# Kernel optimization log

Hardware: AMD Instinct MI355X
Metric: run time of the kernel (lower is better)

Reference implementation:

```python
import jax, jax.numpy as jnp
import numpy as np

N = 50000      # num nodes
E = 400000     # num edges
D = 384        # input_dim
H = 4          # heads
C = 128        # hidden_dim per head
HC = H * C     # 512


def setup_inputs() -> dict:
    key = jax.random.key(0)
    ks = jax.random.split(key, 32)
    w = lambda k, shape: jax.random.normal(k, shape, jnp.float32) * 0.05
    inp = {
        "x": jax.random.normal(ks[0], (N, D), jnp.float32),
        "edge_index": jax.random.randint(ks[1], (2, E), 0, N, dtype=jnp.int32),
    }
    dims = [(D, HC), (HC, HC)]  # layer0 in=384, layer1 in=512
    i = 2
    for l, (din, dout) in enumerate(dims):
        for nm in ["q", "k", "v", "s"]:  # query/key/value/skip linears
            inp[f"{nm}{l}_w"] = w(ks[i], (dout, din)); i += 1
            inp[f"{nm}{l}_b"] = jnp.zeros((dout,), jnp.float32)
    inp["out_w"] = w(ks[i], (D, HC))
    inp["out_b"] = jnp.zeros((D,), jnp.float32)
    return inp


def _transformer_conv(x, src, dst, Wq, bq, Wk, bk, Wv, bv, Ws, bs):
    # PyG TransformerConv, concat=True, root_weight=True, no edge features.
    n = x.shape[0]
    q = (x @ Wq.T + bq).reshape(n, H, C)
    k = (x @ Wk.T + bk).reshape(n, H, C)
    v = (x @ Wv.T + bv).reshape(n, H, C)
    # per-edge attention logits [E, H]; target = dst, source = src
    alpha = (q[dst] * k[src]).sum(-1) / jnp.sqrt(jnp.float32(C))
    m = jax.ops.segment_max(alpha, dst, num_segments=n)
    m = jnp.where(jnp.isfinite(m), m, 0.0)  # nodes with no in-edges
    e = jnp.exp(alpha - m[dst])
    denom = jax.ops.segment_sum(e, dst, num_segments=n)
    a = e / (denom[dst] + 1e-16)             # segment softmax [E, H]
    msg = v[src] * a[:, :, None]             # [E, H, C]
    agg = jax.ops.segment_sum(msg, dst, num_segments=n).reshape(n, HC)
    return agg + x @ Ws.T + bs               # + root/skip connection


def reference(x, edge_index,
              q0_w, q0_b, k0_w, k0_b, v0_w, v0_b, s0_w, s0_b,
              q1_w, q1_b, k1_w, k1_b, v1_w, v1_b, s1_w, s1_b,
              out_w, out_b):
    src, dst = edge_index[0], edge_index[1]
    h = _transformer_conv(x, src, dst, q0_w, q0_b, k0_w, k0_b, v0_w, v0_b, s0_w, s0_b)
    h = jax.nn.relu(h)
    h = _transformer_conv(h, src, dst, q1_w, q1_b, k1_w, k1_b, v1_w, v1_b, s1_w, s1_b)
    h = jax.nn.relu(h)
    return h @ out_w.T + out_b  # [N, D]
```

## Files before the change

kernel.cpp:

```cpp
#include <hip/hip_runtime.h>
#include <hip/hip_bf16.h>

#define NN 50000
#define NE 400000
#define DD 384
#define HC 512

typedef unsigned int u32;
typedef unsigned short u16;
typedef __attribute__((ext_vector_type(8))) short bf16x8;
typedef __attribute__((ext_vector_type(4))) float f32x4;

#define AS1 __attribute__((address_space(1)))
#define AS3 __attribute__((address_space(3)))

__device__ __forceinline__ float bflo(u32 u){ return __uint_as_float(u << 16); }
__device__ __forceinline__ float bfhi(u32 u){ return __uint_as_float(u & 0xFFFF0000u); }
__device__ __forceinline__ u16 f2bf(float f){
    u32 u = __float_as_uint(f);
    return (u16)((u + 0x7FFFu + ((u >> 16) & 1u)) >> 16);
}
__device__ __forceinline__ u32 pack2(float a, float b){
    return (u32)f2bf(a) | ((u32)f2bf(b) << 16);
}

template<int K>
__global__ __launch_bounds__(512)
void gemm_ws(const u16* __restrict__ Ab, const u16* __restrict__ Wb,
             const float* __restrict__ bias,
             u16* __restrict__ oQ, u16* __restrict__ oK,
             u16* __restrict__ oV, u16* __restrict__ oS)
{
    constexpr int NKT  = K / 64;
    constexpr int WCH  = K / 8;
    constexpr int NPAN = (NN + 127) / 128;
    __shared__ char smW[128 * K * 2];
    __shared__ char smA[2][16384];

    const int b   = blockIdx.x;
    const int xcd = b & 7;
    const int idx = b >> 3;
    const int ct  = idx & 15;
    const int rh  = idx >> 4;

    const int tid  = threadIdx.x;
    const int lane = tid & 63;
    const int w    = tid >> 6;
    const int wq   = w >> 1;
    const int wc   = w & 1;
    const int r16  = lane & 15;
    const int kq   = lane >> 4;

    {
        const u16* W0 = Wb + (size_t)ct * 128 * K;
        #pragma unroll
        for (int p = 0; p < (128 * WCH) / 512; ++p) {
            int ci = p * 512 + tid;
            int row = ci / WCH, pc = ci % WCH;
            int lc = (pc & ~7) | ((pc ^ row) & 7);
            __builtin_amdgcn_global_load_lds((const AS1 u32*)(W0 + (size_t)row * K + lc * 8),
                                             (AS3 u32*)(smW + (size_t)ci * 16), 16, 0, 0);
        }
    }

    int np = 0;
    while ((2 * np + rh) * 8 + xcd < NPAN) ++np;
    const int total = np * NKT;

    auto stageA = [&](int t) {
        int jp = t / NKT, kc = t - jp * NKT;
        int m0 = ((2 * jp + rh) * 8 + xcd) * 128;
        #pragma unroll
        for (int p = 0; p < 2; ++p) {
            int ci = p * 512 + tid;
            int row = ci >> 3, pc = ci & 7;
            int lc = pc ^ (row & 7);
            int gr = m0 + row; if (gr >= NN) gr = NN - 1;
            __builtin_amdgcn_global_load_lds((const AS1 u32*)(Ab + (size_t)gr * K + kc * 64 + lc * 8),
                                             (AS3 u32*)(smA[t & 1] + ci * 16), 16, 0, 0);
        }
    };

    stageA(0);
    if (total > 1) stageA(1);

    f32x4 acc[2][4] = {};

    const int qsel = ct >> 2;
    u16* outp = (qsel == 0) ? oQ : (qsel == 1) ? oK : (qsel == 2) ? oV : oS;
    const int cb = (ct & 3) * 128 + wc * 64;
    float bb[4][4];
    #pragma unroll
    for (int ni = 0; ni < 4; ++ni)
        #pragma unroll
        for (int r = 0; r < 4; ++r)
            bb[ni][r] = bias[ct * 128 + wc * 64 + ni * 16 + kq * 4 + r];

    for (int t = 0; t < total; ++t) {
        const int jp = t / NKT, kc = t - jp * NKT;
        if (t + 1 >= total)        { asm volatile("s_waitcnt vmcnt(0)"  ::: "memory"); }
        else if (kc == 0 && t > 0) { asm volatile("s_waitcnt vmcnt(10)" ::: "memory"); }
        else                       { asm volatile("s_waitcnt vmcnt(2)"  ::: "memory"); }
        __builtin_amdgcn_s_barrier();
        __builtin_amdgcn_sched_barrier(0);

        const char* bufA = smA[t & 1];
        #pragma unroll
        for (int kk = 0; kk < 2; ++kk) {
            const int slot = (((kk << 2) + kq) ^ (r16 & 7)) << 4;
            bf16x8 av[2], bv[4];
            #pragma unroll
            for (int i = 0; i < 2; ++i)
                av[i] = *(const bf16x8*)(bufA + (wq * 32 + i * 16 + r16) * 128 + slot);
            #pragma unroll
            for (int i = 0; i < 4; ++i) {
                int rw = wc * 64 + i * 16 + r16;
                bv[i] = *(const bf16x8*)(smW + (size_t)rw * (K * 2) + kc * 128 + slot);
            }
            #pragma unroll
            for (int mi = 0; mi < 2; ++mi)
                #pragma unroll
                for (int ni = 0; ni < 4; ++ni)
                    acc[mi][ni] = __builtin_amdgcn_mfma_f32_16x16x32_bf16(
                        bv[ni], av[mi], acc[mi][ni], 0, 0, 0);
        }

        __builtin_amdgcn_sched_barrier(0);
        __builtin_amdgcn_s_barrier();
        __builtin_amdgcn_sched_barrier(0);

        if (kc == NKT - 1) {
            int m0 = ((2 * jp + rh) * 8 + xcd) * 128;
            #pragma unroll
            for (int mi = 0; mi < 2; ++mi) {
                int gr = m0 + wq * 32 + mi * 16 + r16;
                bool ok = gr < NN;
                #pragma unroll
                for (int ni = 0; ni < 4; ++ni) {
                    uint2 o;
                    o.x = pack2(acc[mi][ni][0] + bb[ni][0], acc[mi][ni][1] + bb[ni][1]);
                    o.y = pack2(acc[mi][ni][2] + bb[ni][2], acc[mi][ni][3] + bb[ni][3]);
                    if (ok) *(uint2*)(outp + (size_t)gr * 512 + cb + ni * 16 + kq * 4) = o;
                    #pragma unroll
                    for (int r = 0; r < 4; ++r) acc[mi][ni][r] = 0.f;
                }
            }
        }
        if (t + 2 < total) stageA(t + 2);
    }
}

template<int K>
__global__ __launch_bounds__(256)
void gemm2ph(const u16* __restrict__ Ab, const u16* __restrict__ Wb,
             const float* __restrict__ bias, float* __restrict__ oF,
             int n, int Ototal, int NT)
{
    constexpr int NKT = K / 64;
    __shared__ char smA[2][16384];
    __shared__ char smB[2][16384];

    const int nb  = gridDim.x;
    const int bd  = blockIdx.x;
    const int q8  = nb >> 3, r8 = nb & 7;
    const int xcd = bd & 7, gg = bd >> 3;
    const int tt  = (xcd < r8 ? xcd * (q8 + 1) : r8 * (q8 + 1) + (xcd - r8) * q8) + gg;
    const int m0  = (tt / NT) * 128;
    const int o0  = (tt % NT) * 128;

    const int tid  = threadIdx.x;
    const int lane = tid & 63;
    const int w    = tid >> 6;
    const int wr   = w >> 1, wc = w & 1;
    const int r16  = lane & 15;
    const int kq   = lane >> 4;

    auto stage = [&](int bf, int kt) {
        #pragma unroll
        for (int p = 0; p < 4; ++p) {
            int ci = p * 256 + tid, row = ci >> 3, pc = ci & 7;
            int lc = pc ^ (row & 7);
            const u16* g = Wb + (size_t)(o0 + row) * K + kt * 64 + lc * 8;
            __builtin_amdgcn_global_load_lds((const AS1 u32*)g,
                                             (AS3 u32*)(smB[bf] + ci * 16), 16, 0, 0);
        }
        #pragma unroll
        for (int p = 0; p < 4; ++p) {
            int ci = p * 256 + tid, row = ci >> 3, pc = ci & 7;
            int lc = pc ^ (row & 7);
            int gr = m0 + row; if (gr >= n) gr = n - 1;
            const u16* g = Ab + (size_t)gr * K + kt * 64 + lc * 8;
            __builtin_amdgcn_global_load_lds((const AS1 u32*)g,
                                             (AS3 u32*)(smA[bf] + ci * 16), 16, 0, 0);
        }
    };

    f32x4 acc[4][4] = {};

    stage(0, 0);
    stage(1, 1);

    for (int kt = 0; kt < NKT; ++kt) {
        if (kt + 1 < NKT) { asm volatile("s_waitcnt vmcnt(8)" ::: "memory"); }
        else             { asm volatile("s_waitcnt vmcnt(0)" ::: "memory"); }
        __builtin_amdgcn_s_barrier();
        __builtin_amdgcn_sched_barrier(0);

        const char* pa = smA[kt & 1] + (wr * 64) * 128;
        const char* pb = smB[kt & 1] + (wc * 64) * 128;
        #pragma unroll
        for (int kk = 0; kk < 2; ++kk) {
            const int slot = (((kk << 2) + kq) ^ (r16 & 7)) << 4;
            bf16x8 av[4], bv[4];
            #pragma unroll
            for (int i = 0; i < 4; ++i) {
                av[i] = *(const bf16x8*)(pa + (i * 16 + r16) * 128 + slot);
                bv[i] = *(const bf16x8*)(pb + (i * 16 + r16) * 128 + slot);
            }
            #pragma unroll
            for (int mi = 0; mi < 4; ++mi)
                #pragma unroll
                for (int ni = 0; ni < 4; ++ni)
                    acc[mi][ni] = __builtin_amdgcn_mfma_f32_16x16x32_bf16(
                        bv[ni], av[mi], acc[mi][ni], 0, 0, 0);
        }

        __builtin_amdgcn_sched_barrier(0);
        __builtin_amdgcn_s_barrier();
        __builtin_amdgcn_sched_barrier(0);
        if (kt + 2 < NKT) stage(kt & 1, kt + 2);
    }

    #pragma unroll
    for (int mi = 0; mi < 4; ++mi) {
        int gr = m0 + wr * 64 + mi * 16 + r16;
        if (gr >= n) continue;
        #pragma unroll
        for (int ni = 0; ni < 4; ++ni) {
            int col = o0 + wc * 64 + ni * 16 + kq * 4;
            float4 o = make_float4(acc[mi][ni][0] + bias[col],
                                   acc[mi][ni][1] + bias[col + 1],
                                   acc[mi][ni][2] + bias[col + 2],
                                   acc[mi][ni][3] + bias[col + 3]);
            *(float4*)(oF + (size_t)gr * Ototal + col) = o;
        }
    }
}

#define XG  2400000
#define W0G 24576
#define W1G 32768
#define WOG 24576
#define CVT_TOTAL (XG + 4*W0G + 4*W1G + WOG)

__global__ __launch_bounds__(256)
void cvt_all(const float* __restrict__ x,
             const float* q0w, const float* k0w, const float* v0w, const float* s0w,
             const float* q1w, const float* k1w, const float* v1w, const float* s1w,
             const float* ow,
             u16* __restrict__ Xb, u16* __restrict__ Wc0,
             u16* __restrict__ Wc1, u16* __restrict__ WcO)
{
    int i = blockIdx.x * 256 + threadIdx.x;
    if (i >= CVT_TOTAL) return;
    const float* s; u16* d; int g;
    if (i < XG) { s = x; d = Xb; g = i; }
    else {
        int j = i - XG;
        if (j < 4 * W0G) {
            int q = j / W0G; g = j - q * W0G;
            s = (q == 0 ? q0w : q == 1 ? k0w : q == 2 ? v0w : s0w);
            d = Wc0 + (size_t)q * W0G * 8;
        } else if ((j -= 4 * W0G) < 4 * W1G) {
            int q = j / W1G; g = j - q * W1G;
            s = (q == 0 ? q1w : q == 1 ? k1w : q == 2 ? v1w : s1w);
            d = Wc1 + (size_t)q * W1G * 8;
        } else { j -= 4 * W1G; s = ow; d = WcO; g = j; }
    }
    float4 f0 = ((const float4*)s)[(size_t)g * 2];
    float4 f1 = ((const float4*)s)[(size_t)g * 2 + 1];
    uint4 o;
    o.x = pack2(f0.x, f0.y); o.y = pack2(f0.z, f0.w);
    o.z = pack2(f1.x, f1.y); o.w = pack2(f1.z, f1.w);
    ((uint4*)d)[g] = o;
}

__global__ __launch_bounds__(256)
void pack_bias(const float* q0, const float* k0, const float* v0, const float* s0,
               const float* q1, const float* k1, const float* v1, const float* s1,
               const float* ob, float* __restrict__ dst)
{
    int i = blockIdx.x * 256 + threadIdx.x;
    if (i >= 4480) return;
    float v;
    if (i < 2048) {
        int j = i & 511, q = i >> 9;
        v = (q == 0 ? q0 : q == 1 ? k0 : q == 2 ? v0 : s0)[j];
    } else if (i < 4096) {
        int j = i - 2048; int q = j >> 9; j &= 511;
        v = (q == 0 ? q1 : q == 1 ? k1 : q == 2 ? v1 : s1)[j];
    } else {
        v = ob[i - 4096];
    }
    dst[i] = v;
}

__global__ __launch_bounds__(256)
void zero_deg(int* __restrict__ deg)
{
    int i = blockIdx.x * 256 + threadIdx.x;
    if (i < NN) deg[i] = 0;
}

__global__ __launch_bounds__(256)
void hist_dst(const int* __restrict__ dst, int* __restrict__ deg)
{
    int e = blockIdx.x * 256 + threadIdx.x;
    if (e < NE) atomicAdd(&deg[dst[e]], 1);
}

__global__ __launch_bounds__(1024)
void scan_deg(const int* __restrict__ deg, int* __restrict__ rowptr,
              int* __restrict__ cursor)
{
    __shared__ int wsum[16];
    const int tid = threadIdx.x, lane = tid & 63, wid = tid >> 6;
    int carry = 0;
    for (int base = 0; base < NN; base += 1024) {
        int i = base + tid;
        int orig = (i < NN) ? deg[i] : 0;
        int v = orig;
        #pragma unroll
        for (int off = 1; off < 64; off <<= 1) {
            int t = __shfl_up(v, off, 64);
            if (lane >= off) v += t;
        }
        if (lane == 63) wsum[wid] = v;
        __syncthreads();
        if (wid == 0) {
            int s = (lane < 16) ? wsum[lane] : 0;
            #pragma unroll
            for (int off = 1; off < 16; off <<= 1) {
                int t = __shfl_up(s, off, 16);
                if ((lane & 15) >= off) s += t;
            }
            if (lane < 16) wsum[lane] = s;
        }
        __syncthreads();
        int woff  = (wid == 0) ? 0 : wsum[wid - 1];
        int total = wsum[15];
        int excl  = carry + woff + (v - orig);
        if (i < NN) { rowptr[i] = excl; cursor[i] = excl; }
        carry += total;
        __syncthreads();
    }
    if (tid == 0) rowptr[NN] = NE;
}

__global__ __launch_bounds__(256)
void scatter_edges(const int* __restrict__ src, const int* __restrict__ dst,
                   int* __restrict__ cursor, int* __restrict__ esrc_ord)
{
    int e = blockIdx.x * 256 + threadIdx.x;
    if (e >= NE) return;
    int pos = atomicAdd(&cursor[dst[e]], 1);
    esrc_ord[pos] = src[e];
}

__global__ __launch_bounds__(256)
void node_attn(const u16* __restrict__ Qb, const u16* __restrict__ Kb,
               const u16* __restrict__ Vb, const int* __restrict__ rowptr,
               const int* __restrict__ esrc, const u16* __restrict__ skipb,
               u16* __restrict__ outb)
{
    int d = blockIdx.x * 4 + (threadIdx.x >> 6);
    if (d >= NN) return;
    int lane = threadIdx.x & 63;

    uint4 qv = *((const uint4*)(Qb + (size_t)d * HC) + lane);
    float q[8] = { bflo(qv.x), bfhi(qv.x), bflo(qv.y), bfhi(qv.y),
                   bflo(qv.z), bfhi(qv.z), bflo(qv.w), bfhi(qv.w) };

    int beg = rowptr[d], end = rowptr[d + 1];
    float m = -INFINITY, den = 0.f;
    float acc[8] = {};

    if (beg < end) {
        int s0 = esrc[beg];
        uint4 kv = *((const uint4*)(Kb + (size_t)s0 * HC) + lane);
        uint4 vv = *((const uint4*)(Vb + (size_t)s0 * HC) + lane);

        for (int i = beg; i < end; ++i) {
            uint4 kc = kv, vc = vv;
            if (i + 1 < end) {
                int sn = esrc[i + 1];
                kv = *((const uint4*)(Kb + (size_t)sn * HC) + lane);
                vv = *((const uint4*)(Vb + (size_t)sn * HC) + lane);
            }
            float sum = q[0] * bflo(kc.x) + q[1] * bfhi(kc.x)
                      + q[2] * bflo(kc.y) + q[3] * bfhi(kc.y)
                      + q[4] * bflo(kc.z) + q[5] * bfhi(kc.z)
                      + q[6] * bflo(kc.w) + q[7] * bfhi(kc.w);
            #pragma unroll
            for (int off = 1; off < 16; off <<= 1) sum += __shfl_xor(sum, off, 64);
            float alpha = sum * 0.08838834764831845f;

            float mnew  = fmaxf(m, alpha);
            float scale = __expf(m - mnew);
            float p     = __expf(alpha - mnew);
            den = den * scale + p;

            acc[0] = acc[0] * scale + p * bflo(vc.x);
            acc[1] = acc[1] * scale + p * bfhi(vc.x);
            acc[2] = acc[2] * scale + p * bflo(vc.y);
            acc[3] = acc[3] * scale + p * bfhi(vc.y);
            acc[4] = acc[4] * scale + p * bflo(vc.z);
            acc[5] = acc[5] * scale + p * bfhi(vc.z);
            acc[6] = acc[6] * scale + p * bflo(vc.w);
            acc[7] = acc[7] * scale + p * bfhi(vc.w);
            m = mnew;
        }
    }

    float inv = 1.f / (den + 1e-16f);
    size_t base = (size_t)d * HC + lane * 8;
    uint4 sv = *((const uint4*)(skipb + base));
    float sk[8] = { bflo(sv.x), bfhi(sv.x), bflo(sv.y), bfhi(sv.y),
                    bflo(sv.z), bfhi(sv.z), bflo(sv.w), bfhi(sv.w) };
    uint4 o;
    o.x = pack2(fmaxf(acc[0] * inv + sk[0], 0.f), fmaxf(acc[1] * inv + sk[1], 0.f));
    o.y = pack2(fmaxf(acc[2] * inv + sk[2], 0.f), fmaxf(acc[3] * inv + sk[3], 0.f));
    o.z = pack2(fmaxf(acc[4] * inv + sk[4], 0.f), fmaxf(acc[5] * inv + sk[5], 0.f));
    o.w = pack2(fmaxf(acc[6] * inv + sk[6], 0.f), fmaxf(acc[7] * inv + sk[7], 0.f));
    *(uint4*)(outb + base) = o;
}

extern "C" void kernel_launch(void* const* d_in, const int* in_sizes, int n_in,
                              void* d_out, int out_size, void* d_ws, size_t ws_size,
                              hipStream_t stream)
{
    const float* x   = (const float*)d_in[0];
    const int* ei    = (const int*)d_in[1];
    const int* esrc  = ei;
    const int* edst  = ei + NE;
    const float* q0w = (const float*)d_in[2];  const float* q0b = (const float*)d_in[3];
    const float* k0w = (const float*)d_in[4];  const float* k0b = (const float*)d_in[5];
    const float* v0w = (const float*)d_in[6];  const float* v0b = (const float*)d_in[7];
    const float* s0w = (const float*)d_in[8];  const float* s0b = (const float*)d_in[9];
    const float* q1w = (const float*)d_in[10]; const float* q1b = (const float*)d_in[11];
    const float* k1w = (const float*)d_in[12]; const float* k1b = (const float*)d_in[13];
    const float* v1w = (const float*)d_in[14]; const float* v1b = (const float*)d_in[15];
    const float* s1w = (const float*)d_in[16]; const float* s1b = (const float*)d_in[17];
    const float* ow  = (const float*)d_in[18]; const float* obs = (const float*)d_in[19];

    char* p = (char*)d_ws;
    auto take = [&](size_t bytes) { void* r = (void*)p; p += (bytes + 255) & ~(size_t)255; return r; };
    u16*   Qb     = (u16*)take((size_t)NN * HC * 2);
    u16*   Vb     = (u16*)take((size_t)NN * HC * 2);
    u16*   Hb     = (u16*)take((size_t)NN * HC * 2);
    u16*   Sb     = (u16*)take((size_t)NN * HC * 2);
    u16*   Xb     = (u16*)take((size_t)NN * DD * 2);
    u16*   Wc0    = (u16*)take((size_t)2048 * DD * 2);
    u16*   Wc1    = (u16*)take((size_t)2048 * HC * 2);
    u16*   WcO    = (u16*)take((size_t)DD * HC * 2);
    float* barena = (float*)take(4480 * 4);

    char* dob = (char*)d_out;
    u16* Kb       = (u16*)dob;
    int* deg      = (int*)(dob + 51200000);
    int* rowptr   = (int*)(dob + 51400192);
    int* cursor   = (int*)(dob + 51600384);
    int* esrc_ord = (int*)(dob + 51800576);

    dim3 blk(256);
    int gN   = (NN + 255) / 256;
    int gE   = (NE + 255) / 256;
    int gnod = (NN + 3) / 4;
    const int NPAN = (NN + 127) / 128;
    int go = NPAN * 3;

    pack_bias<<<(4480 + 255) / 256, blk, 0, stream>>>(q0b, k0b, v0b, s0b,
                                                      q1b, k1b, v1b, s1b, obs, barena);
    cvt_all<<<(CVT_TOTAL + 255) / 256, blk, 0, stream>>>(x,
        q0w, k0w, v0w, s0w, q1w, k1w, v1w, s1w, ow, Xb, Wc0, Wc1, WcO);

    zero_deg      <<<gN, blk, 0, stream>>>(deg);
    hist_dst      <<<gE, blk, 0, stream>>>(edst, deg);
    scan_deg      <<<1, 1024, 0, stream>>>(deg, rowptr, cursor);
    scatter_edges <<<gE, blk, 0, stream>>>(esrc, edst, cursor, esrc_ord);

    gemm_ws<DD><<<256, 512, 0, stream>>>(Xb, Wc0, barena, Qb, Kb, Vb, Sb);
    node_attn<<<gnod, blk, 0, stream>>>(Qb, Kb, Vb, rowptr, esrc_ord, Sb, Hb);

    gemm_ws<HC><<<256, 512, 0, stream>>>(Hb, Wc1, barena + 2048, Qb, Kb, Vb, Sb);
    node_attn<<<gnod, blk, 0, stream>>>(Qb, Kb, Vb, rowptr, esrc_ord, Sb, Hb);

    gemm2ph<HC><<<go, blk, 0, stream>>>(Hb, WcO, barena + 4096,
                                        (float*)d_out, NN, 384, 3);
}
```

Before: 792.3 us.

## Enlarge weight-stationary GEMM row panel to 256 with 32-wide K steps

The weight-stationary QKVS GEMM now processes 256-row A panels in 32-wide K chunks with a new LDS swizzle. Each wave computes a 4x4 MFMA tile instead of 2x4, which raises reuse of the resident weight tile per A load. MFMA operand order is swapped in both GEMMs, so epilogues write scalar values down columns instead of packed vectors along rows. The swap changes the store pattern to strided scalar writes, which risks worse write coalescing and adds register pressure from the larger accumulator.

```diff
diff --git a/kernel.cpp b/kernel.cpp
--- a/kernel.cpp
+++ b/kernel.cpp
@@ -31,9 +31,9 @@
              u16* __restrict__ oQ, u16* __restrict__ oK,
              u16* __restrict__ oV, u16* __restrict__ oS)
 {
-    constexpr int NKT  = K / 64;
+    constexpr int NKC  = K / 32;
     constexpr int WCH  = K / 8;
-    constexpr int NPAN = (NN + 127) / 128;
+    constexpr int NPAN = (NN + 255) / 256;
     __shared__ char smW[128 * K * 2];
     __shared__ char smA[2][16384];
 
@@ -46,7 +46,7 @@
     const int tid  = threadIdx.x;
     const int lane = tid & 63;
     const int w    = tid >> 6;
-    const int wq   = w >> 1;
+    const int wr   = w >> 1;
     const int wc   = w & 1;
     const int r16  = lane & 15;
     const int kq   = lane >> 4;
@@ -65,18 +65,18 @@
 
     int np = 0;
     while ((2 * np + rh) * 8 + xcd < NPAN) ++np;
-    const int total = np * NKT;
+    const int total = np * NKC;
 
     auto stageA = [&](int t) {
-        int jp = t / NKT, kc = t - jp * NKT;
-        int m0 = ((2 * jp + rh) * 8 + xcd) * 128;
+        int jp = t / NKC, kc = t - jp * NKC;
+        int m0 = ((2 * jp + rh) * 8 + xcd) * 256;
         #pragma unroll
         for (int p = 0; p < 2; ++p) {
             int ci = p * 512 + tid;
-            int row = ci >> 3, pc = ci & 7;
-            int lc = pc ^ (row & 7);
+            int row = ci >> 2, pc = ci & 3;
+            int lc = (pc - (row >> 1)) & 3;
             int gr = m0 + row; if (gr >= NN) gr = NN - 1;
-            __builtin_amdgcn_global_load_lds((const AS1 u32*)(Ab + (size_t)gr * K + kc * 64 + lc * 8),
+            __builtin_amdgcn_global_load_lds((const AS1 u32*)(Ab + (size_t)gr * K + kc * 32 + lc * 8),
                                              (AS3 u32*)(smA[t & 1] + ci * 16), 16, 0, 0);
         }
     };
@@ -84,69 +84,68 @@
     stageA(0);
     if (total > 1) stageA(1);
 
-    f32x4 acc[2][4] = {};
+    f32x4 acc[4][4] = {};
 
     const int qsel = ct >> 2;
     u16* outp = (qsel == 0) ? oQ : (qsel == 1) ? oK : (qsel == 2) ? oV : oS;
     const int cb = (ct & 3) * 128 + wc * 64;
-    float bb[4][4];
+    float bv4[4];
     #pragma unroll
-    for (int ni = 0; ni < 4; ++ni)
-        #pragma unroll
-        for (int r = 0; r < 4; ++r)
-            bb[ni][r] = bias[ct * 128 + wc * 64 + ni * 16 + kq * 4 + r];
+    for (int ni = 0; ni < 4; ++ni) bv4[ni] = bias[ct * 128 + wc * 64 + ni * 16 + r16];
 
     for (int t = 0; t < total; ++t) {
-        const int jp = t / NKT, kc = t - jp * NKT;
-        if (t + 1 >= total)        { asm volatile("s_waitcnt vmcnt(0)"  ::: "memory"); }
-        else if (kc == 0 && t > 0) { asm volatile("s_waitcnt vmcnt(10)" ::: "memory"); }
-        else                       { asm volatile("s_waitcnt vmcnt(2)"  ::: "memory"); }
+        const int jp = t / NKC, kc = t - jp * NKC;
+        if (t + 1 >= total)          { asm volatile("s_waitcnt vmcnt(0)"  ::: "memory"); }
+        else if (kc <= 1 && t > 1)   { asm volatile("s_waitcnt vmcnt(63)" ::: "memory"); }
+        else                         { asm volatile("s_waitcnt vmcnt(2)"  ::: "memory"); }
         __builtin_amdgcn_s_barrier();
         __builtin_amdgcn_sched_barrier(0);
 
         const char* bufA = smA[t & 1];
-        #pragma unroll
-        for (int kk = 0; kk < 2; ++kk) {
-            const int slot = (((kk << 2) + kq) ^ (r16 & 7)) << 4;
-            bf16x8 av[2], bv[4];
-            #pragma unroll
-            for (int i = 0; i < 2; ++i)
-                av[i] = *(const bf16x8*)(bufA + (wq * 32 + i * 16 + r16) * 128 + slot);
-            #pragma unroll
-            for (int i = 0; i < 4; ++i) {
-                int rw = wc * 64 + i * 16 + r16;
-                bv[i] = *(const bf16x8*)(smW + (size_t)rw * (K * 2) + kc * 128 + slot);
-            }
-            #pragma unroll
-            for (int mi = 0; mi < 2; ++mi)
-                #pragma unroll
-                for (int ni = 0; ni < 4; ++ni)
-                    acc[mi][ni] = __builtin_amdgcn_mfma_f32_16x16x32_bf16(
-                        bv[ni], av[mi], acc[mi][ni], 0, 0, 0);
-        }
+        const int c = kc * 4 + kq;
+        const int wbase = (c & ~7) << 4;
+        bf16x8 av[4], bv[4];
+        #pragma unroll
+        for (int i = 0; i < 4; ++i) {
+            int rowA = wr * 64 + i * 16 + r16;
+            av[i] = *(const bf16x8*)(bufA + rowA * 64 + (((kq + (rowA >> 1)) & 3) << 4));
+        }
+        #pragma unroll
+        for (int i = 0; i < 4; ++i) {
+            int rowW = wc * 64 + i * 16 + r16;
+            bv[i] = *(const bf16x8*)(smW + (size_t)rowW * (K * 2) + wbase
+                                     + (((c ^ rowW) & 7) << 4));
+        }
+        #pragma unroll
+        for (int mi = 0; mi < 4; ++mi)
+            #pragma unroll
+            for (int ni = 0; ni < 4; ++ni)
+                acc[mi][ni] = __builtin_amdgcn_mfma_f32_16x16x32_bf16(
+                    av[mi], bv[ni], acc[mi][ni], 0, 0, 0);
 
         __builtin_amdgcn_sched_barrier(0);
         __builtin_amdgcn_s_barrier();
         __builtin_amdgcn_sched_barrier(0);
 
-        if (kc == NKT - 1) {
-            int m0 = ((2 * jp + rh) * 8 + xcd) * 128;
-            #pragma unroll
-            for (int mi = 0; mi < 2; ++mi) {
-                int gr = m0 + wq * 32 + mi * 16 + r16;
-                bool ok = gr < NN;
+        if (t + 2 < total) stageA(t + 2);
+
+        if (kc == NKC - 1) {
+            int m0 = ((2 * jp + rh) * 8 + xcd) * 256;
+            #pragma unroll
+            for (int mi = 0; mi < 4; ++mi) {
                 #pragma unroll
                 for (int ni = 0; ni < 4; ++ni) {
-                    uint2 o;
-                    o.x = pack2(acc[mi][ni][0] + bb[ni][0], acc[mi][ni][1] + bb[ni][1]);
-                    o.y = pack2(acc[mi][ni][2] + bb[ni][2], acc[mi][ni][3] + bb[ni][3]);
-                    if (ok) *(uint2*)(outp + (size_t)gr * 512 + cb + ni * 16 + kq * 4) = o;
+                    int col = cb + ni * 16 + r16;
+                    float bb = bv4[ni];
                     #pragma unroll
-                    for (int r = 0; r < 4; ++r) acc[mi][ni][r] = 0.f;
+                    for (int r = 0; r < 4; ++r) {
+                        int gr = m0 + wr * 64 + mi * 16 + kq * 4 + r;
+                        if (gr < NN) outp[(size_t)gr * 512 + col] = f2bf(acc[mi][ni][r] + bb);
+                        acc[mi][ni][r] = 0.f;
+                    }
                 }
             }
         }
-        if (t + 2 < total) stageA(t + 2);
     }
 }
 
@@ -174,6 +173,7 @@
     const int wr   = w >> 1, wc = w & 1;
     const int r16  = lane & 15;
     const int kq   = lane >> 4;
+    const int swz  = (r16 & 7) << 4;
 
     auto stage = [&](int bf, int kt) {
         #pragma unroll
@@ -210,19 +210,19 @@
         const char* pb = smB[kt & 1] + (wc * 64) * 128;
         #pragma unroll
         for (int kk = 0; kk < 2; ++kk) {
-            const int slot = (((kk << 2) + kq) ^ (r16 & 7)) << 4;
+            const int kb = kk * 64 + kq * 16;
             bf16x8 av[4], bv[4];
             #pragma unroll
             for (int i = 0; i < 4; ++i) {
-                av[i] = *(const bf16x8*)(pa + (i * 16 + r16) * 128 + slot);
-                bv[i] = *(const bf16x8*)(pb + (i * 16 + r16) * 128 + slot);
+                av[i] = *(const bf16x8*)(pa + (i * 16 + r16) * 128 + (kb ^ swz));
+                bv[i] = *(const bf16x8*)(pb + (i * 16 + r16) * 128 + (kb ^ swz));
             }
             #pragma unroll
             for (int mi = 0; mi < 4; ++mi)
                 #pragma unroll
                 for (int ni = 0; ni < 4; ++ni)
                     acc[mi][ni] = __builtin_amdgcn_mfma_f32_16x16x32_bf16(
-                        bv[ni], av[mi], acc[mi][ni], 0, 0, 0);
+                        av[mi], bv[ni], acc[mi][ni], 0, 0, 0);
         }
 
         __builtin_amdgcn_sched_barrier(0);
@@ -231,19 +231,18 @@
         if (kt + 2 < NKT) stage(kt & 1, kt + 2);
     }
 
+    const int cbo = o0 + wc * 64;
     #pragma unroll
-    for (int mi = 0; mi < 4; ++mi) {
-        int gr = m0 + wr * 64 + mi * 16 + r16;
-        if (gr >= n) continue;
-        #pragma unroll
-        for (int ni = 0; ni < 4; ++ni) {
-            int col = o0 + wc * 64 + ni * 16 + kq * 4;
-            float4 o = make_float4(acc[mi][ni][0] + bias[col],
-                                   acc[mi][ni][1] + bias[col + 1],
-                                   acc[mi][ni][2] + bias[col + 2],
-                                   acc[mi][ni][3] + bias[col + 3]);
-            *(float4*)(oF + (size_t)gr * Ototal + col) = o;
-        }
+    for (int ni = 0; ni < 4; ++ni) {
+        int col = cbo + ni * 16 + r16;
+        float bb = bias[col];
+        #pragma unroll
+        for (int mi = 0; mi < 4; ++mi)
+            #pragma unroll
+            for (int r = 0; r < 4; ++r) {
+                int gr = m0 + wr * 64 + mi * 16 + kq * 4 + r;
+                if (gr < n) oF[(size_t)gr * Ototal + col] = acc[mi][ni][r] + bb;
+            }
     }
 }
 
```

After: 777.0 us. No clear change (-1.9%).
